# Kernel tuning notes

Measured on AMD Instinct MI355X. Metric: run time of the kernel, lower is better.

## Reference

```python
import jax, jax.numpy as jnp
import numpy as np

B, T, DIM, H, HD = 2, 2048, 1024, 8, 128
ATTN_SCALE = 0.12  # attn_args.attn_scale (modded-nanogpt constant)
F32_EPS = float(np.finfo(np.float32).eps)  # F.rms_norm default eps


def ste_round(x):
    # straight-through round (round_grad_pt): identity gradient
    return x + jax.lax.stop_gradient(jnp.round(x) - x)


def quantized_linear(x, num_bits=8, eps=1e-5):
    num_steps = (2 ** num_bits - 1) // 2  # 127
    xnmin = jnp.minimum(jnp.min(x, -1, keepdims=True), -eps)
    xpmax = jnp.maximum(jnp.max(x, -1, keepdims=True), eps)
    xp = ste_round(x / xpmax * num_steps) / num_steps * xpmax
    xn = ste_round(x / xnmin * num_steps) / num_steps * xnmin
    return jnp.where(x >= 0, xp, xn)


def ternary_quantize_mean_special(w):
    # w: [3, hdim, dim]; per-leading-slice scale
    s = jnp.maximum(jnp.mean(jnp.mean(jnp.abs(w), -1, keepdims=True), -2, keepdims=True), 1e-5)
    return s * jnp.clip(ste_round(w / s), -1.0, 1.0)


def ternary_quantize(w):
    s = jnp.maximum(jnp.mean(jnp.abs(w)), 1e-5)
    return s * jnp.clip(ste_round(w / s), -1.0, 1.0)


def rmsnorm(x):
    return x * jax.lax.rsqrt(jnp.mean(x * x, -1, keepdims=True) + F32_EPS)


def rotary(x, cos, sin):
    # x: [B,T,H,HD]; cos,sin: [T, HD//2]
    x1, x2 = jnp.split(x, 2, axis=-1)
    c = cos[None, :, None, :]
    s = sin[None, :, None, :]
    return jnp.concatenate([x1 * c + x2 * s, -x1 * s + x2 * c], axis=-1)


def setup_inputs() -> dict:
    key = jax.random.key(0)
    ks = jax.random.split(key, 5)
    x = jax.random.normal(ks[0], (B, T, DIM), jnp.float32)
    ve = jax.random.normal(ks[1], (B, T, DIM), jnp.float32)
    sa_lambdas = jnp.array([0.5, 0.5], jnp.float32)
    inv_freq = 1.0 / (10000.0 ** (np.arange(0, HD, 2, dtype=np.float32) / HD))
    ang = np.arange(T, dtype=np.float32)[:, None] * inv_freq[None, :]
    cos = jnp.asarray(np.cos(ang), jnp.float32)
    sin = jnp.asarray(np.sin(ang), jnp.float32)
    bound = (3.0 ** 0.5) * 0.5 * DIM ** (-0.5)
    qkvo_w = jax.random.uniform(ks[2], (4, H * HD, DIM), jnp.float32, -bound, bound)
    gate_w = 0.1 * jax.random.normal(ks[3], (H, 12), jnp.float32)
    return {"x": x, "ve": ve, "sa_lambdas": sa_lambdas, "cos": cos, "sin": sin,
            "qkvo_w": qkvo_w, "gate_w": gate_w}


def reference(x, ve, sa_lambdas, cos, sin, qkvo_w, gate_w):
    # pre-activation int8 fake-quant (ENABLE_ATTN_PRE_ACT_QUANTIZATION)
    xq = quantized_linear(x, num_bits=8)
    # ternary-quantized QKV weights (ENABLE_ATTN_QUANTIZATION)
    w_qkv = ternary_quantize_mean_special(qkvo_w[:3]).reshape(3 * H * HD, DIM)
    qkv = jnp.einsum('btd,ed->bte', xq, w_qkv).reshape(B, T, 3 * H, HD)
    q, k, v = qkv[:, :, :H], qkv[:, :, H:2 * H], qkv[:, :, 2 * H:]
    q, k = rmsnorm(q), rmsnorm(k)
    q, k = rotary(q, cos, sin), rotary(k, cos, sin)
    v = sa_lambdas[0] * v + sa_lambdas[1] * ve.reshape(v.shape)
    # q/k int8 fake-quant (ENABLE_ATTN_ACT_QUANTIZATION)
    q = quantized_linear(q, num_bits=8)
    k = quantized_linear(k, num_bits=8)
    # causal SDPA with explicit scale
    scores = jnp.einsum('bqhd,bkhd->bhqk', q, k) * ATTN_SCALE
    mask = jnp.tril(jnp.ones((T, T), bool))
    scores = jnp.where(mask[None, None], scores, -jnp.inf)
    p = jax.nn.softmax(scores, axis=-1)
    y = jnp.einsum('bhqk,bkhd->bqhd', p, v)  # [B,T,H,HD]
    # sigmoid gate from first 12 features of (quantized) x
    gate = jax.nn.sigmoid(jnp.einsum('btf,hf->bth', xq[..., :12], gate_w))
    y = (y * gate[..., None]).reshape(B, T, H * HD)
    # ternary-quantized output projection (ENABLE_ATTN_PROJ_QUANTIZATION)
    w_o = ternary_quantize(qkvo_w[3])
    return jnp.einsum('bte,de->btd', y, w_o)
```

## Files before the change

### kernel.cpp

```cpp
#include <hip/hip_runtime.h>
#include <hip/hip_bf16.h>
#include <cstddef>
#include <cstdint>

#define B_    2
#define T_    2048
#define DIM_  1024
#define H_    8
#define HD_   128
#define BT_   (B_*T_)
#define E3_   (3*H_*HD_)
#define F32_EPS_ 1.1920929e-07f
#define QSC_  0.17312340490667562f

typedef __attribute__((ext_vector_type(8))) short bh8_t;
typedef __attribute__((ext_vector_type(4))) float f32x4_t;
typedef __attribute__((ext_vector_type(16))) float f32x16_t;
typedef __attribute__((ext_vector_type(4))) unsigned short us4_t;

__device__ inline unsigned short bf16r(float f) {
    unsigned u = __builtin_bit_cast(unsigned, f);
    u = (u + 0x7fffu + ((u >> 16) & 1u)) >> 16;
    return (unsigned short)u;
}
__device__ inline float b2f(unsigned short u) {
    return __builtin_bit_cast(float, (unsigned)u << 16);
}
__device__ inline unsigned cvtpk(float a, float b) {
    unsigned r;
    asm("v_cvt_pk_bf16_f32 %0, %1, %2" : "=v"(r) : "v"(a), "v"(b));
    return r;
}
__device__ inline void gl16(const unsigned short* g, unsigned short* l) {
    __builtin_amdgcn_global_load_lds((const __attribute__((address_space(1))) void*)g,
                                     (__attribute__((address_space(3))) void*)l, 16, 0, 0);
}

__global__ __launch_bounds__(256) void absmean1_kernel(const float* __restrict__ w, float* __restrict__ partial) {
    int blk = blockIdx.x;
    size_t off = (size_t)blk * 4096;
    __shared__ float red[256];
    int tid = threadIdx.x;
    float acc = 0.f;
    const float* p = w + off + tid*16;
    #pragma unroll
    for (int j = 0; j < 4; j++) {
        float4 v = *(const float4*)(p + j*4);
        acc += fabsf(v.x) + fabsf(v.y) + fabsf(v.z) + fabsf(v.w);
    }
    red[tid] = acc; __syncthreads();
    for (int s = 128; s > 0; s >>= 1) { if (tid < s) red[tid] += red[tid+s]; __syncthreads(); }
    if (tid == 0) partial[blk] = red[0];
}

__global__ __launch_bounds__(256) void prep_kernel(const float* __restrict__ w, const float* __restrict__ partial,
                                                   const float* __restrict__ x, const float* __restrict__ gw,
                                                   unsigned short* __restrict__ wq,
                                                   unsigned short* __restrict__ xqb, float* __restrict__ gate,
                                                   float* __restrict__ scales) {
    __shared__ float red[256];
    __shared__ float x12[12];
    int bid = blockIdx.x;
    int tid = threadIdx.x;
    if (bid < 2048) {
        int m = bid >> 9;
        red[tid] = partial[m*256 + tid]; __syncthreads();
        for (int s = 128; s > 0; s >>= 1) { if (tid < s) red[tid] += red[tid+s]; __syncthreads(); }
        float sm = fmaxf(red[0] / (float)(DIM_*DIM_), 1e-5f);
        float inv = 1.f / sm;
        int base = (bid * 256 + tid) * 8;
        unsigned short out[8];
        float4 v0 = *(const float4*)(w + base);
        float4 v1 = *(const float4*)(w + base + 4);
        float t[8] = {v0.x, v0.y, v0.z, v0.w, v1.x, v1.y, v1.z, v1.w};
        #pragma unroll
        for (int j = 0; j < 8; j++) {
            float r = rintf(t[j] * inv);
            r = fminf(1.f, fmaxf(-1.f, r));
            out[j] = (r == 0.f) ? 0 : (r > 0.f ? 0x3F80 : 0xBF80);
        }
        *(int4*)(wq + base) = *(const int4*)out;
    } else if (bid < 2048 + BT_) {
        int row = bid - 2048;
        const float* xr = x + (size_t)row * DIM_;
        unsigned short* qr = xqb + (size_t)row * DIM_;
        int w_ = tid >> 6, l = tid & 63;
        float v[4];
        float mn = 1e30f, mx = -1e30f;
        #pragma unroll
        for (int i = 0; i < 4; i++) {
            v[i] = xr[i*256 + tid];
            mn = fminf(mn, v[i]); mx = fmaxf(mx, v[i]);
        }
        #pragma unroll
        for (int off = 1; off < 64; off <<= 1) {
            mn = fminf(mn, __shfl_xor(mn, off));
            mx = fmaxf(mx, __shfl_xor(mx, off));
        }
        if (l == 0) { red[w_] = mn; red[4 + w_] = mx; }
        __syncthreads();
        mn = fminf(fminf(red[0], red[1]), fminf(red[2], red[3]));
        mx = fmaxf(fmaxf(red[4], red[5]), fmaxf(red[6], red[7]));
        float p = fmaxf(mx, 1e-5f);
        float n = fminf(mn, -1e-5f);
        #pragma unroll
        for (int i = 0; i < 4; i++) {
            int gi = i*256 + tid;
            float xv = v[i];
            float sc = (xv >= 0.f) ? p : n;
            float q = rintf(xv / sc * 127.f) / 127.f * sc;
            qr[gi] = bf16r(q);
            if (gi < 12) x12[gi] = q;
        }
        __syncthreads();
        if (tid < H_) {
            float acc = 0.f;
            #pragma unroll
            for (int f = 0; f < 12; f++) acc += x12[f] * gw[tid*12 + f];
            gate[(size_t)row * H_ + tid] = 1.f / (1.f + expf(-acc));
        }
    } else {
        int m = bid - (2048 + BT_);
        red[tid] = partial[m*256 + tid]; __syncthreads();
        for (int s = 128; s > 0; s >>= 1) { if (tid < s) red[tid] += red[tid+s]; __syncthreads(); }
        if (tid == 0) scales[m] = fmaxf(red[0] / (float)(DIM_*DIM_), 1e-5f);
    }
}

template<int MT, bool OBF>
__global__ __launch_bounds__(256) void gemm_bf16_kernel(const unsigned short* __restrict__ A,
                                                        const unsigned short* __restrict__ Bm,
                                                        const float* __restrict__ sw, int sbase,
                                                        void* __restrict__ Cv, int M, int N, int K) {
    __shared__ __align__(16) unsigned short As[MT*32*64];
    __shared__ __align__(16) unsigned short Bs[128*64];
    int bm = blockIdx.y * (MT*32), bn = blockIdx.x * 128;
    int tid = threadIdx.x;
    int w = tid >> 6, l = tid & 63;
    int wr = w >> 1, wc = w & 1;
    int lg = l >> 4, lq = l & 15;
    f32x4_t acc[MT][4];
    #pragma unroll
    for (int mt = 0; mt < MT; mt++)
        #pragma unroll
        for (int nt = 0; nt < 4; nt++) acc[mt][nt] = (f32x4_t)0.f;

    for (int k0 = 0; k0 < K; k0 += 64) {
        #pragma unroll
        for (int i = 0; i < MT; i++) {
            int ob = (i*4 + w) << 10;
            int o  = ob + (l << 4);
            int row = o >> 7;
            int lcn = ((o >> 4) & 7) ^ (row & 7);
            gl16(A + (size_t)(bm+row)*K + k0 + lcn*8, (unsigned short*)As + (ob >> 1));
        }
        #pragma unroll
        for (int i = 0; i < 4; i++) {
            int ob = (i*4 + w) << 10;
            int o  = ob + (l << 4);
            int row = o >> 7;
            int lcn = ((o >> 4) & 7) ^ (row & 7);
            gl16(Bm + (size_t)(bn+row)*K + k0 + lcn*8, (unsigned short*)Bs + (ob >> 1));
        }
        __syncthreads();
        #pragma unroll
        for (int kk = 0; kk < 2; kk++) {
            bh8_t af[MT], bf[4];
            #pragma unroll
            for (int mt = 0; mt < MT; mt++) {
                int r = wr*(MT*16) + mt*16 + lq;
                int j = kk*4 + lg;
                af[mt] = *(const bh8_t*)(As + r*64 + (((j ^ (r & 7)))<<3));
            }
            #pragma unroll
            for (int nt = 0; nt < 4; nt++) {
                int r = wc*64 + nt*16 + lq;
                int j = kk*4 + lg;
                bf[nt] = *(const bh8_t*)(Bs + r*64 + (((j ^ (r & 7)))<<3));
            }
            #pragma unroll
            for (int mt = 0; mt < MT; mt++)
                #pragma unroll
                for (int nt = 0; nt < 4; nt++)
                    acc[mt][nt] = __builtin_amdgcn_mfma_f32_16x16x32_bf16(af[mt], bf[nt], acc[mt][nt], 0, 0, 0);
        }
        __syncthreads();
    }
    #pragma unroll
    for (int nt = 0; nt < 4; nt++) {
        int col = bn + wc*64 + nt*16 + lq;
        float s = sw[sbase + (col >> 10)];
        #pragma unroll
        for (int mt = 0; mt < MT; mt++) {
            int row = bm + wr*(MT*16) + mt*16 + lg*4;
            #pragma unroll
            for (int r = 0; r < 4; r++) {
                if constexpr (OBF)
                    ((unsigned short*)Cv)[(size_t)(row + r)*N + col] = bf16r(acc[mt][nt][r] * s);
                else
                    ((float*)Cv)[(size_t)(row + r)*N + col] = acc[mt][nt][r] * s;
            }
        }
    }
}

__global__ __launch_bounds__(256) void qkv_post_tv_kernel(const unsigned short* __restrict__ qkvb,
                                                          const float* __restrict__ ve,
                                                          const float* __restrict__ lam,
                                                          const float* __restrict__ cosb, const float* __restrict__ sinb,
                                                          unsigned short* __restrict__ Qb, unsigned short* __restrict__ Kb,
                                                          unsigned short* __restrict__ VT) {
    __shared__ unsigned short L[64][80];
    int bid = blockIdx.x;
    int tid = threadIdx.x;
    if (bid < BT_) {
        int bt = bid;
        int b = bt >> 11, t = bt & (T_ - 1);
        int w = tid >> 6, l = tid & 63;
        const unsigned short* base = qkvb + (size_t)bt * E3_;
        float cc = cosb[(size_t)t*64 + l], ss = sinb[(size_t)t*64 + l];
        #pragma unroll
        for (int i = 0; i < 4; i++) {
            int part = w*4 + i;
            const unsigned short* row = base + part*HD_;
            float x1 = b2f(row[l]), x2 = b2f(row[l+64]);
            float ssq = x1*x1 + x2*x2;
            #pragma unroll
            for (int off = 1; off < 64; off <<= 1) ssq += __shfl_xor(ssq, off);
            float rms = 1.0f / sqrtf(ssq / 128.0f + F32_EPS_);
            x1 *= rms; x2 *= rms;
            float o1 = x1*cc + x2*ss;
            float o2 = -x1*ss + x2*cc;
            float mn = fminf(o1, o2), mx = fmaxf(o1, o2);
            #pragma unroll
            for (int off = 1; off < 64; off <<= 1) {
                mn = fminf(mn, __shfl_xor(mn, off));
                mx = fmaxf(mx, __shfl_xor(mx, off));
            }
            float p = fmaxf(mx, 1e-5f);
            float n = fminf(mn, -1e-5f);
            float s1 = (o1 >= 0.f) ? p : n;
            float s2 = (o2 >= 0.f) ? p : n;
            float q1 = rintf(o1 / s1 * 127.f) / 127.f * s1;
            float q2 = rintf(o2 / s2 * 127.f) / 127.f * s2;
            if (part < 8) {
                unsigned short* dst = Qb + ((size_t)(b*H_+part)*T_ + t)*HD_;
                dst[l] = bf16r(QSC_ * q1); dst[l + 64] = bf16r(QSC_ * q2);
            } else {
                unsigned short* dst = Kb + ((size_t)(b*H_+part-8)*T_ + t)*HD_;
                dst[l] = bf16r(q1); dst[l + 64] = bf16r(q2);
            }
        }
    } else {
        int r0 = bid - BT_;
        int tt = r0 & 31;
        int dt = (r0 >> 5) & 1;
        int bh = r0 >> 6;
        int b = bh >> 3, h = bh & 7;
        float l0 = lam[0], l1 = lam[1];
        #pragma unroll
        for (int i = 0; i < 2; i++) {
            int c = tid + i*256;
            int r = c >> 3, dc = c & 7;
            size_t bt = (size_t)(b*T_ + tt*64 + r);
            union { int4 v; unsigned short q[8]; } u;
            u.v = *(const int4*)(qkvb + bt*E3_ + (16 + h)*HD_ + dt*64 + dc*8);
            float4 va = *(const float4*)(ve + bt*DIM_ + h*HD_ + dt*64 + dc*8);
            float4 vb = *(const float4*)(ve + bt*DIM_ + h*HD_ + dt*64 + dc*8 + 4);
            float vv[8] = {va.x, va.y, va.z, va.w, vb.x, vb.y, vb.z, vb.w};
            unsigned short mix[8];
            #pragma unroll
            for (int k = 0; k < 8; k++) mix[k] = bf16r(l0*b2f(u.q[k]) + l1*vv[k]);
            *(int4*)(&L[r][dc*8]) = *(const int4*)mix;
        }
        __syncthreads();
        #pragma unroll
        for (int i = 0; i < 2; i++) {
            int c = tid + i*256;
            int r = c >> 3, tc = c & 7;
            unsigned short tmp[8];
            #pragma unroll
            for (int jj = 0; jj < 8; jj++) tmp[jj] = L[tc*8+jj][r];
            *(int4*)(VT + ((size_t)bh*HD_ + dt*64 + r)*T_ + tt*64 + tc*8) = *(const int4*)tmp;
        }
    }
}

__global__ __launch_bounds__(256) void attn_kernel(const unsigned short* __restrict__ Qb,
                                                   const unsigned short* __restrict__ Kb,
                                                   const unsigned short* __restrict__ VT,
                                                   const float* __restrict__ gate,
                                                   unsigned short* __restrict__ Yb) {
    __shared__ __align__(16) unsigned char SMEM[65536];
    int id = blockIdx.x;
    int bh = id & 15;
    int qi = id >> 4;
    int qt = (qi < 16) ? (31 - qi) : (qi - 16);
    int b = bh >> 3, h = bh & 7;
    int tid = threadIdx.x;
    int w = tid >> 6, l = tid & 63;
    int qsub = w >> 1, qq = w & 1;
    int hh = l >> 5, l5 = l & 31;
    int qrow = qsub*32 + l5;
    int qg = qt*64 + qrow;

    const unsigned short* Kbase = Kb + (size_t)bh*T_*HD_;
    const unsigned short* Vbase = VT + (size_t)bh*HD_*T_;
    const unsigned short* Qg = Qb + ((size_t)bh*T_ + (size_t)qt*64) * HD_;

    bh8_t qf[8];
    #pragma unroll
    for (int ks = 0; ks < 8; ks++)
        qf[ks] = *(const bh8_t*)(Qg + (size_t)qrow*HD_ + ks*16 + hh*8);

    int nr = qt + 1;

    f32x16_t o0 = (f32x16_t)0.f, o1 = (f32x16_t)0.f, o2 = (f32x16_t)0.f, o3 = (f32x16_t)0.f;
    float mrun = -1e20f, lrun = 0.f;

#define STAGE(BI, J) { \
    unsigned short* kb_ = (unsigned short*)(SMEM + (BI)*16384); \
    unsigned short* vb_ = (unsigned short*)(SMEM + 32768 + (BI)*16384); \
    _Pragma("unroll") \
    for (int i_ = 0; i_ < 4; i_++) { \
        int ob_ = (i_*4 + w) << 10; \
        int o_  = ob_ + (l << 4); \
        int rk_ = o_ >> 8; \
        int lk_ = ((o_ >> 4) & 15) ^ (rk_ & 15); \
        gl16(Kbase + (size_t)((J)*64 + rk_)*HD_ + lk_*8, kb_ + (ob_ >> 1)); \
        int rv_ = o_ >> 7; \
        int lv_ = ((o_ >> 4) & 7) ^ (rv_ & 7); \
        gl16(Vbase + (size_t)rv_*T_ + (J)*64 + lv_*8, vb_ + (ob_ >> 1)); \
    } }

    STAGE(0, 0);
    for (int j = 0; j < nr; j++) {
        if (j + 1 < nr) {
            STAGE((j+1) & 1, j+1);
            asm volatile("s_waitcnt vmcnt(8)" ::: "memory");
        } else {
            asm volatile("s_waitcnt vmcnt(0)" ::: "memory");
        }
        __builtin_amdgcn_s_barrier();
        asm volatile("" ::: "memory");
        const unsigned short* kb = (const unsigned short*)(SMEM + (j&1)*16384);
        const unsigned short* vb = (const unsigned short*)(SMEM + 32768 + (j&1)*16384);
        int kvb = j*64 + qq*32;
        if (kvb <= qt*64 + qsub*32 + 31) {
            f32x16_t s = (f32x16_t)0.f;
            int krow = qq*32 + l5;
            __builtin_amdgcn_s_setprio(1);
            #pragma unroll
            for (int ks = 0; ks < 8; ks++) {
                int c = (ks*2 + hh) ^ (krow & 15);
                bh8_t kf = *(const bh8_t*)(kb + krow*128 + c*8);
                s = __builtin_amdgcn_mfma_f32_32x32x16_bf16(kf, qf[ks], s, 0, 0, 0);
            }
            __builtin_amdgcn_s_setprio(0);
            if (kvb + 31 > qt*64 + qsub*32) {
                #pragma unroll
                for (int r = 0; r < 16; r++) {
                    int key = kvb + (r & 3) + 8*(r >> 2) + 4*hh;
                    if (key > qg) s[r] = -1e30f;
                }
            }
            float t8[8], t4[4];
            #pragma unroll
            for (int r = 0; r < 8; r++) t8[r] = fmaxf(s[2*r], s[2*r+1]);
            #pragma unroll
            for (int r = 0; r < 4; r++) t4[r] = fmaxf(t8[2*r], t8[2*r+1]);
            float tm = fmaxf(fmaxf(t4[0], t4[1]), fmaxf(t4[2], t4[3]));
            tm = fmaxf(tm, __shfl_xor(tm, 32));
            if (!__all(tm - mrun <= 8.f)) {
                float mnew = fmaxf(mrun, tm);
                float scf = __builtin_amdgcn_exp2f(mrun - mnew);
                lrun *= scf;
                o0 *= scf; o1 *= scf; o2 *= scf; o3 *= scf;
                mrun = mnew;
            }
            float p[16];
            #pragma unroll
            for (int r = 0; r < 16; r++) p[r] = __builtin_amdgcn_exp2f(s[r] - mrun);
            #pragma unroll
            for (int r = 0; r < 8; r++) t8[r] = p[2*r] + p[2*r+1];
            #pragma unroll
            for (int r = 0; r < 4; r++) t4[r] = t8[2*r] + t8[2*r+1];
            float ls = (t4[0] + t4[1]) + (t4[2] + t4[3]);
            ls += __shfl_xor(ls, 32);
            lrun += ls;
            unsigned u0 = cvtpk(p[0], p[1]),   u1 = cvtpk(p[2], p[3]);
            unsigned u2 = cvtpk(p[4], p[5]),   u3 = cvtpk(p[6], p[7]);
            unsigned u4 = cvtpk(p[8], p[9]),   u5 = cvtpk(p[10], p[11]);
            unsigned u6 = cvtpk(p[12], p[13]), u7 = cvtpk(p[14], p[15]);
            unsigned x0 = (unsigned)__shfl_xor((int)u0, 32), x1 = (unsigned)__shfl_xor((int)u1, 32);
            unsigned x2 = (unsigned)__shfl_xor((int)u2, 32), x3 = (unsigned)__shfl_xor((int)u3, 32);
            unsigned x4 = (unsigned)__shfl_xor((int)u4, 32), x5 = (unsigned)__shfl_xor((int)u5, 32);
            unsigned x6 = (unsigned)__shfl_xor((int)u6, 32), x7 = (unsigned)__shfl_xor((int)u7, 32);
            union { bh8_t v; unsigned uu[4]; } B0, B1;
            B0.uu[0] = hh ? x2 : u0;  B0.uu[1] = hh ? x3 : u1;
            B0.uu[2] = hh ? u2 : x0;  B0.uu[3] = hh ? u3 : x1;
            B1.uu[0] = hh ? x6 : u4;  B1.uu[1] = hh ? x7 : u5;
            B1.uu[2] = hh ? u6 : x4;  B1.uu[3] = hh ? u7 : x5;
            __builtin_amdgcn_s_setprio(1);
#define PV_STEP(DT, OACC) { \
    int vrow = DT*32 + l5; \
    bh8_t vf0 = *(const bh8_t*)(vb + vrow*64 + (((qq*4 + hh) ^ (vrow & 7))<<3)); \
    OACC = __builtin_amdgcn_mfma_f32_32x32x16_bf16(vf0, B0.v, OACC, 0, 0, 0); \
    bh8_t vf1 = *(const bh8_t*)(vb + vrow*64 + (((qq*4 + 2 + hh) ^ (vrow & 7))<<3)); \
    OACC = __builtin_amdgcn_mfma_f32_32x32x16_bf16(vf1, B1.v, OACC, 0, 0, 0); }
            PV_STEP(0, o0) PV_STEP(1, o1) PV_STEP(2, o2) PV_STEP(3, o3)
#undef PV_STEP
            __builtin_amdgcn_s_setprio(0);
        }
        asm volatile("s_waitcnt lgkmcnt(0)" ::: "memory");
        __builtin_amdgcn_s_barrier();
        asm volatile("" ::: "memory");
    }

    f32x16_t oA[4] = {o0, o1, o2, o3};
    float* OB = (float*)SMEM;
    float* ML = (float*)(SMEM + 32768);
    unsigned short* YS = (unsigned short*)(SMEM + 33280);
    if (qq != 0) {
        float* obuf = OB + (size_t)qsub * 4096;
        #pragma unroll
        for (int dt = 0; dt < 4; dt++)
            #pragma unroll
            for (int g = 0; g < 4; g++) {
                f32x4_t v4;
                #pragma unroll
                for (int e = 0; e < 4; e++) v4[e] = oA[dt][g*4+e];
                int ch = (dt*4 + g) ^ (l & 7);
                *(f32x4_t*)(obuf + l*64 + ch*4) = v4;
            }
        if (hh == 0) {
            ML[(qsub*32 + l5)*2]     = mrun;
            ML[(qsub*32 + l5)*2 + 1] = lrun;
        }
    }
    __syncthreads();
    if (qq == 0) {
        float mb = ML[(qsub*32 + l5)*2];
        float lb = ML[(qsub*32 + l5)*2 + 1];
        float mN = fmaxf(mrun, mb);
        float fa = __builtin_amdgcn_exp2f(mrun - mN), fb = __builtin_amdgcn_exp2f(mb - mN);
        const float* obuf = OB + (size_t)qsub * 4096;
        #pragma unroll
        for (int dt = 0; dt < 4; dt++)
            #pragma unroll
            for (int g = 0; g < 4; g++) {
                int ch = (dt*4 + g) ^ (l & 7);
                f32x4_t v4 = *(const f32x4_t*)(obuf + l*64 + ch*4);
                #pragma unroll
                for (int e = 0; e < 4; e++)
                    oA[dt][g*4+e] = oA[dt][g*4+e]*fa + v4[e]*fb;
            }
        lrun = lrun*fa + lb*fb;
        float gv = gate[((size_t)b*T_ + (size_t)qg)*H_ + h];
        float inv = gv / lrun;
        #pragma unroll
        for (int dt = 0; dt < 4; dt++)
            #pragma unroll
            for (int g = 0; g < 4; g++) {
                unsigned short pk4[4];
                #pragma unroll
                for (int e = 0; e < 4; e++) pk4[e] = bf16r(oA[dt][g*4+e] * inv);
                int ch = (dt*4 + g) ^ (qrow & 7);
                *(us4_t*)(YS + (size_t)qrow*128 + ch*8 + hh*4) = *(const us4_t*)pk4;
            }
    }
    __syncthreads();
    #pragma unroll
    for (int i = 0; i < 4; i++) {
        int idx = tid + i*256;
        int r = idx >> 4, scn = idx & 15;
        int lcn = scn ^ (r & 7);
        int4 v = *(const int4*)(YS + (size_t)r*128 + scn*8);
        *(int4*)(Yb + (size_t)(b*T_ + qt*64 + r)*DIM_ + h*HD_ + lcn*8) = v;
    }
#undef STAGE
}

extern "C" void kernel_launch(void* const* d_in, const int* in_sizes, int n_in,
                              void* d_out, int out_size, void* d_ws, size_t ws_size,
                              hipStream_t stream) {
    const float* x    = (const float*)d_in[0];
    const float* ve   = (const float*)d_in[1];
    const float* lam  = (const float*)d_in[2];
    const float* cosb = (const float*)d_in[3];
    const float* sinb = (const float*)d_in[4];
    const float* qkvo = (const float*)d_in[5];
    const float* gw   = (const float*)d_in[6];

    char* ws = (char*)d_ws;
    float* scales  = (float*)ws;
    float* partial = scales + 16;
    unsigned short* WQb  = (unsigned short*)(ws + (1<<13));
    unsigned short* XQb  = WQb + (size_t)4*DIM_*DIM_;
    unsigned short* QKVb = XQb + (size_t)BT_*DIM_;
    float* GT = (float*)(QKVb + (size_t)BT_*E3_);
    unsigned short* Qb = (unsigned short*)(GT + (size_t)BT_*H_);
    unsigned short* Kb = Qb + (size_t)B_*H_*T_*HD_;
    unsigned short* VT = Kb + (size_t)B_*H_*T_*HD_;
    unsigned short* Yb = QKVb;

    absmean1_kernel<<<1024, 256, 0, stream>>>(qkvo, partial);
    prep_kernel<<<2048 + BT_ + 4, 256, 0, stream>>>(qkvo, partial, x, gw, WQb, XQb, GT, scales);
    gemm_bf16_kernel<4, true><<<dim3(E3_/128, BT_/128), 256, 0, stream>>>(XQb, WQb, scales, 0, QKVb, BT_, E3_, DIM_);
    qkv_post_tv_kernel<<<BT_ + 1024, 256, 0, stream>>>(QKVb, ve, lam, cosb, sinb, Qb, Kb, VT);
    attn_kernel<<<512, 256, 0, stream>>>(Qb, Kb, VT, GT, Yb);
    gemm_bf16_kernel<2, false><<<dim3(DIM_/128, BT_/64), 256, 0, stream>>>(Yb, WQb + (size_t)3*DIM_*DIM_, scales, 3,
                                                                           (float*)d_out, BT_, DIM_, DIM_);
}
```

Before: 136.8 us.

## Defer softmax and PV MFMA by one iteration to overlap with loads

Software-pipelines the attention loop. Each tile's QK scores and V fragments are saved in registers, and the softmax plus PV MFMAs run during the next iteration, after the next tile's global loads are issued and before waiting on them. The goal is to hide the latency of global-to-LDS loads and of the barrier behind the softmax math. In exchange the kernel holds 8 more bh8 V fragments and a 16-float score vector live across iterations, which raises register pressure and may lower occupancy.

```diff
diff --git a/kernel.cpp b/kernel.cpp
--- a/kernel.cpp
+++ b/kernel.cpp
@@ -303,6 +303,7 @@
     int hh = l >> 5, l5 = l & 31;
     int qrow = qsub*32 + l5;
     int qg = qt*64 + qrow;
+    int qwbase = qt*64 + qsub*32;
 
     const unsigned short* Kbase = Kb + (size_t)bh*T_*HD_;
     const unsigned short* Vbase = VT + (size_t)bh*HD_*T_;
@@ -317,6 +318,11 @@
 
     f32x16_t o0 = (f32x16_t)0.f, o1 = (f32x16_t)0.f, o2 = (f32x16_t)0.f, o3 = (f32x16_t)0.f;
     float mrun = -1e20f, lrun = 0.f;
+
+    f32x16_t sp;
+    bh8_t vreg[8];
+    int pend_kvb = 0;
+    bool havePend = false;
 
 #define STAGE(BI, J) { \
     unsigned short* kb_ = (unsigned short*)(SMEM + (BI)*16384); \
@@ -333,10 +339,70 @@
         gl16(Vbase + (size_t)rv_*T_ + (J)*64 + lv_*8, vb_ + (ob_ >> 1)); \
     } }
 
+#define DO_PEND() { \
+    if (pend_kvb + 31 > qwbase) { \
+        _Pragma("unroll") \
+        for (int r = 0; r < 16; r++) { \
+            int key = pend_kvb + (r & 3) + 8*(r >> 2) + 4*hh; \
+            if (key > qg) sp[r] = -1e30f; \
+        } \
+    } \
+    float t8[8], t4[4]; \
+    _Pragma("unroll") \
+    for (int r = 0; r < 8; r++) t8[r] = fmaxf(sp[2*r], sp[2*r+1]); \
+    _Pragma("unroll") \
+    for (int r = 0; r < 4; r++) t4[r] = fmaxf(t8[2*r], t8[2*r+1]); \
+    float tm = fmaxf(fmaxf(t4[0], t4[1]), fmaxf(t4[2], t4[3])); \
+    tm = fmaxf(tm, __shfl_xor(tm, 32)); \
+    if (!__all(tm - mrun <= 8.f)) { \
+        float mnew = fmaxf(mrun, tm); \
+        float scf = __builtin_amdgcn_exp2f(mrun - mnew); \
+        lrun *= scf; \
+        o0 *= scf; o1 *= scf; o2 *= scf; o3 *= scf; \
+        mrun = mnew; \
+    } \
+    float pp[16]; \
+    _Pragma("unroll") \
+    for (int r = 0; r < 16; r++) pp[r] = __builtin_amdgcn_exp2f(sp[r] - mrun); \
+    _Pragma("unroll") \
+    for (int r = 0; r < 8; r++) t8[r] = pp[2*r] + pp[2*r+1]; \
+    _Pragma("unroll") \
+    for (int r = 0; r < 4; r++) t4[r] = t8[2*r] + t8[2*r+1]; \
+    float ls = (t4[0] + t4[1]) + (t4[2] + t4[3]); \
+    ls += __shfl_xor(ls, 32); \
+    lrun += ls; \
+    unsigned u0 = cvtpk(pp[0], pp[1]),   u1 = cvtpk(pp[2], pp[3]); \
+    unsigned u2 = cvtpk(pp[4], pp[5]),   u3 = cvtpk(pp[6], pp[7]); \
+    unsigned u4 = cvtpk(pp[8], pp[9]),   u5 = cvtpk(pp[10], pp[11]); \
+    unsigned u6 = cvtpk(pp[12], pp[13]), u7 = cvtpk(pp[14], pp[15]); \
+    unsigned x0 = (unsigned)__shfl_xor((int)u0, 32), x1 = (unsigned)__shfl_xor((int)u1, 32); \
+    unsigned x2 = (unsigned)__shfl_xor((int)u2, 32), x3 = (unsigned)__shfl_xor((int)u3, 32); \
+    unsigned x4 = (unsigned)__shfl_xor((int)u4, 32), x5 = (unsigned)__shfl_xor((int)u5, 32); \
+    unsigned x6 = (unsigned)__shfl_xor((int)u6, 32), x7 = (unsigned)__shfl_xor((int)u7, 32); \
+    union { bh8_t v; unsigned uu[4]; } B0, B1; \
+    B0.uu[0] = hh ? x2 : u0;  B0.uu[1] = hh ? x3 : u1; \
+    B0.uu[2] = hh ? u2 : x0;  B0.uu[3] = hh ? u3 : x1; \
+    B1.uu[0] = hh ? x6 : u4;  B1.uu[1] = hh ? x7 : u5; \
+    B1.uu[2] = hh ? u6 : x4;  B1.uu[3] = hh ? u7 : x5; \
+    __builtin_amdgcn_s_setprio(1); \
+    o0 = __builtin_amdgcn_mfma_f32_32x32x16_bf16(vreg[0], B0.v, o0, 0, 0, 0); \
+    o0 = __builtin_amdgcn_mfma_f32_32x32x16_bf16(vreg[1], B1.v, o0, 0, 0, 0); \
+    o1 = __builtin_amdgcn_mfma_f32_32x32x16_bf16(vreg[2], B0.v, o1, 0, 0, 0); \
+    o1 = __builtin_amdgcn_mfma_f32_32x32x16_bf16(vreg[3], B1.v, o1, 0, 0, 0); \
+    o2 = __builtin_amdgcn_mfma_f32_32x32x16_bf16(vreg[4], B0.v, o2, 0, 0, 0); \
+    o2 = __builtin_amdgcn_mfma_f32_32x32x16_bf16(vreg[5], B1.v, o2, 0, 0, 0); \
+    o3 = __builtin_amdgcn_mfma_f32_32x32x16_bf16(vreg[6], B0.v, o3, 0, 0, 0); \
+    o3 = __builtin_amdgcn_mfma_f32_32x32x16_bf16(vreg[7], B1.v, o3, 0, 0, 0); \
+    __builtin_amdgcn_s_setprio(0); \
+}
+
     STAGE(0, 0);
     for (int j = 0; j < nr; j++) {
         if (j + 1 < nr) {
             STAGE((j+1) & 1, j+1);
+        }
+        if (havePend) { DO_PEND(); havePend = false; }
+        if (j + 1 < nr) {
             asm volatile("s_waitcnt vmcnt(8)" ::: "memory");
         } else {
             asm volatile("s_waitcnt vmcnt(0)" ::: "memory");
@@ -346,7 +412,7 @@
         const unsigned short* kb = (const unsigned short*)(SMEM + (j&1)*16384);
         const unsigned short* vb = (const unsigned short*)(SMEM + 32768 + (j&1)*16384);
         int kvb = j*64 + qq*32;
-        if (kvb <= qt*64 + qsub*32 + 31) {
+        if (kvb <= qwbase + 31) {
             f32x16_t s = (f32x16_t)0.f;
             int krow = qq*32 + l5;
             __builtin_amdgcn_s_setprio(1);
@@ -357,65 +423,21 @@
                 s = __builtin_amdgcn_mfma_f32_32x32x16_bf16(kf, qf[ks], s, 0, 0, 0);
             }
             __builtin_amdgcn_s_setprio(0);
-            if (kvb + 31 > qt*64 + qsub*32) {
-                #pragma unroll
-                for (int r = 0; r < 16; r++) {
-                    int key = kvb + (r & 3) + 8*(r >> 2) + 4*hh;
-                    if (key > qg) s[r] = -1e30f;
-                }
-            }
-            float t8[8], t4[4];
-            #pragma unroll
-            for (int r = 0; r < 8; r++) t8[r] = fmaxf(s[2*r], s[2*r+1]);
-            #pragma unroll
-            for (int r = 0; r < 4; r++) t4[r] = fmaxf(t8[2*r], t8[2*r+1]);
-            float tm = fmaxf(fmaxf(t4[0], t4[1]), fmaxf(t4[2], t4[3]));
-            tm = fmaxf(tm, __shfl_xor(tm, 32));
-            if (!__all(tm - mrun <= 8.f)) {
-                float mnew = fmaxf(mrun, tm);
-                float scf = __builtin_amdgcn_exp2f(mrun - mnew);
-                lrun *= scf;
-                o0 *= scf; o1 *= scf; o2 *= scf; o3 *= scf;
-                mrun = mnew;
-            }
-            float p[16];
-            #pragma unroll
-            for (int r = 0; r < 16; r++) p[r] = __builtin_amdgcn_exp2f(s[r] - mrun);
-            #pragma unroll
-            for (int r = 0; r < 8; r++) t8[r] = p[2*r] + p[2*r+1];
-            #pragma unroll
-            for (int r = 0; r < 4; r++) t4[r] = t8[2*r] + t8[2*r+1];
-            float ls = (t4[0] + t4[1]) + (t4[2] + t4[3]);
-            ls += __shfl_xor(ls, 32);
-            lrun += ls;
-            unsigned u0 = cvtpk(p[0], p[1]),   u1 = cvtpk(p[2], p[3]);
-            unsigned u2 = cvtpk(p[4], p[5]),   u3 = cvtpk(p[6], p[7]);
-            unsigned u4 = cvtpk(p[8], p[9]),   u5 = cvtpk(p[10], p[11]);
-            unsigned u6 = cvtpk(p[12], p[13]), u7 = cvtpk(p[14], p[15]);
-            unsigned x0 = (unsigned)__shfl_xor((int)u0, 32), x1 = (unsigned)__shfl_xor((int)u1, 32);
-            unsigned x2 = (unsigned)__shfl_xor((int)u2, 32), x3 = (unsigned)__shfl_xor((int)u3, 32);
-            unsigned x4 = (unsigned)__shfl_xor((int)u4, 32), x5 = (unsigned)__shfl_xor((int)u5, 32);
-            unsigned x6 = (unsigned)__shfl_xor((int)u6, 32), x7 = (unsigned)__shfl_xor((int)u7, 32);
-            union { bh8_t v; unsigned uu[4]; } B0, B1;
-            B0.uu[0] = hh ? x2 : u0;  B0.uu[1] = hh ? x3 : u1;
-            B0.uu[2] = hh ? u2 : x0;  B0.uu[3] = hh ? u3 : x1;
-            B1.uu[0] = hh ? x6 : u4;  B1.uu[1] = hh ? x7 : u5;
-            B1.uu[2] = hh ? u6 : x4;  B1.uu[3] = hh ? u7 : x5;
-            __builtin_amdgcn_s_setprio(1);
-#define PV_STEP(DT, OACC) { \
-    int vrow = DT*32 + l5; \
-    bh8_t vf0 = *(const bh8_t*)(vb + vrow*64 + (((qq*4 + hh) ^ (vrow & 7))<<3)); \
-    OACC = __builtin_amdgcn_mfma_f32_32x32x16_bf16(vf0, B0.v, OACC, 0, 0, 0); \
-    bh8_t vf1 = *(const bh8_t*)(vb + vrow*64 + (((qq*4 + 2 + hh) ^ (vrow & 7))<<3)); \
-    OACC = __builtin_amdgcn_mfma_f32_32x32x16_bf16(vf1, B1.v, OACC, 0, 0, 0); }
-            PV_STEP(0, o0) PV_STEP(1, o1) PV_STEP(2, o2) PV_STEP(3, o3)
-#undef PV_STEP
-            __builtin_amdgcn_s_setprio(0);
+            sp = s;
+            #pragma unroll
+            for (int dt = 0; dt < 4; dt++) {
+                int vrow = dt*32 + l5;
+                vreg[dt*2]   = *(const bh8_t*)(vb + vrow*64 + (((qq*4 + hh) ^ (vrow & 7))<<3));
+                vreg[dt*2+1] = *(const bh8_t*)(vb + vrow*64 + (((qq*4 + 2 + hh) ^ (vrow & 7))<<3));
+            }
+            pend_kvb = kvb;
+            havePend = true;
         }
         asm volatile("s_waitcnt lgkmcnt(0)" ::: "memory");
         __builtin_amdgcn_s_barrier();
         asm volatile("" ::: "memory");
     }
+    if (havePend) DO_PEND();
 
     f32x16_t oA[4] = {o0, o1, o2, o3};
     float* OB = (float*)SMEM;
@@ -479,6 +501,7 @@
         *(int4*)(Yb + (size_t)(b*T_ + qt*64 + r)*DIM_ + h*HD_ + lcn*8) = v;
     }
 #undef STAGE
+#undef DO_PEND
 }
 
 extern "C" void kernel_launch(void* const* d_in, const int* in_sizes, int n_in,
```

Result: slower. 153.9 us (+12.5%).
